# Performance work log

Measured on AMD Instinct MI355X. Metric: run time of the kernel, lower is better.

Reference implementation:

```python
import jax, jax.numpy as jnp
import numpy as np

NX, NY = 384, 384
H = 1e-4
DT = 5e-9
NT = 192
STRIDE = 4
RHO = 1610.0
F0 = 2.0e6
T0 = 4e-7
AMP = 1e10
GAUSS_A = 5e6

C11_INIT, C22_INIT, C12_INIT = 1.3074e11, 1.15e10, 1.049e10
C16_INIT, C26_INIT, C66_INIT = 3.067e10, 3.75e9, 1.477e10
B11 = (5e10, 2.5e11); B22 = (5e9, 5e10); B12 = (5e9, 5e10)
B16 = (0.0, 6e10); B26 = (0.0, 2e10); B66 = (5e9, 3e10)


def setup_inputs() -> dict:
    # log-parameter fields, constant-initialized as in the module __init__
    full = lambda v: jnp.full((1, NX, NY), np.log(v), dtype=jnp.float32)
    log_C11 = full(C11_INIT)
    log_C22 = full(C22_INIT)
    log_C12 = full(C12_INIT)
    log_C16 = full(abs(C16_INIT) + 1e6)
    log_C26 = full(abs(C26_INIT) + 1e6)
    log_C66 = full(C66_INIT)
    # Gaussian point-load distribution centered at domain center
    Lx, Ly = H * (NX - 1), H * (NY - 1)
    x = np.linspace(-Lx / 2, Lx / 2, NX)
    y = np.linspace(-Ly / 2, Ly / 2, NY)
    X, Y = np.meshgrid(x, y, indexing='ij')
    gauss = (GAUSS_A / np.pi) * np.exp(-GAUSS_A * (X ** 2 + Y ** 2))
    # Ricker wavelet source signal over nt steps
    t = np.arange(NT) * DT
    tau = t - T0
    pft2 = (np.pi * F0 * tau) ** 2
    sig = AMP * (1.0 - 2.0 * pft2) * np.exp(-pft2)
    return {
        'log_C11': log_C11, 'log_C12': log_C12, 'log_C16': log_C16,
        'log_C22': log_C22, 'log_C26': log_C26, 'log_C66': log_C66,
        'gaussian_dist': jnp.asarray(gauss, dtype=jnp.float32),
        'source_signal': jnp.asarray(sig, dtype=jnp.float32),
    }


def _stencils(u, hinv2):
    # u: (B, nx, ny). Zero padding == fixed (u=0) boundary, matching conv2d_fixed.
    up = jnp.pad(u, ((0, 0), (1, 1), (1, 1)))
    d2x = (up[:, :-2, 1:-1] - 2.0 * u + up[:, 2:, 1:-1]) * hinv2
    d2y = (up[:, 1:-1, :-2] - 2.0 * u + up[:, 1:-1, 2:]) * hinv2
    dxy = 0.25 * (up[:, :-2, :-2] - up[:, :-2, 2:] - up[:, 2:, :-2] + up[:, 2:, 2:]) * hinv2
    return d2x, d2y, dxy


def _simulate(log_C11, log_C12, log_C16, log_C22, log_C26, log_C66,
              gaussian_dist, source_signal):
    clip = lambda lc, b: jnp.clip(jnp.exp(lc), b[0], b[1])
    C11 = clip(log_C11, B11); C22 = clip(log_C22, B22); C12 = clip(log_C12, B12)
    C16 = clip(log_C16, B16); C26 = clip(log_C26, B26); C66 = clip(log_C66, B66)
    hinv2 = jnp.float32(1.0 / (H * H))
    dt2 = jnp.float32(DT * DT)
    g = gaussian_dist[None]  # (1, nx, ny)
    C12p66 = C12 + C66

    def step(carry, sig_t):
        ux1, uy1, ux2, uy2 = carry
        dxx_x, dyy_x, dxy_x = _stencils(ux1, hinv2)
        dxx_y, dyy_y, dxy_y = _stencils(uy1, hinv2)
        Lux = (C11 * dxx_x + C66 * dyy_x + C12p66 * dxy_y
               + 2.0 * C16 * dxy_x + C16 * dxx_y + C26 * dyy_y)
        Luy = (C66 * dxx_y + C22 * dyy_y + C12p66 * dxy_x
               + C16 * dxx_x + C26 * dyy_x + 2.0 * C26 * dxy_y)
        # Ricker point source on the y-component (source_component='y')
        ax = Lux / RHO
        ay = (Luy + sig_t * g) / RHO
        ux_new = 2.0 * ux1 - ux2 + dt2 * ax
        uy_new = 2.0 * uy1 - uy2 + dt2 * ay
        return (ux_new, uy_new, ux1, uy1), (ux_new, uy_new)

    z = jnp.zeros((1, NX, NY), dtype=jnp.float32)
    _, (ux_all, uy_all) = jax.lax.scan(step, (z, z, z, z), source_signal)
    # subsample by primary_time_stride -> (1, nt//stride, nx, ny)
    ux_f = jnp.transpose(ux_all[STRIDE - 1::STRIDE], (1, 0, 2, 3))
    uy_f = jnp.transpose(uy_all[STRIDE - 1::STRIDE], (1, 0, 2, 3))
    return jnp.stack([ux_f, uy_f])  # (2, 1, nt_out, nx, ny)


def reference(log_C11, log_C12, log_C16, log_C22, log_C26, log_C66,
              gaussian_dist, source_signal):
    return _simulate(log_C11, log_C12, log_C16, log_C22, log_C26, log_C66,
                     gaussian_dist, source_signal)
```

## Files before the change

### kernel.cpp

```cpp
#include <hip/hip_runtime.h>


typedef float v2f __attribute__((ext_vector_type(2)));

#define NXg 384
#define NYg 384
#define NPT (NXg * NYg)
#define NFRAMES 48

#define OWN 24
#define HALO 12
#define TS 48
#define KSTEPS 12
#define NLAUNCH 16

#define H_   1e-4
#define DT_  5e-9
#define RHO_ 1610.0

#define B11_LO 5e10f
#define B11_HI 2.5e11f
#define B22_LO 5e9f
#define B22_HI 5e10f
#define B12_LO 5e9f
#define B12_HI 5e10f
#define B16_LO 0.0f
#define B16_HI 6e10f
#define B26_LO 0.0f
#define B26_HI 2e10f
#define B66_LO 5e9f
#define B66_HI 3e10f

static __device__ __constant__ float kScale  = (float)(DT_ * DT_ / (H_ * H_) / RHO_);
static __device__ __constant__ float kSrcScl = (float)(DT_ * DT_ / RHO_);

__device__ __forceinline__ float clipf(float v, float lo, float hi) {
    return fminf(fmaxf(v, lo), hi);
}
__device__ __forceinline__ v2f vfma(v2f a, v2f b, v2f c) {
    return __builtin_elementwise_fma(a, b, c);
}
__device__ __forceinline__ v2f vbc(float s) { v2f r; r[0] = s; r[1] = s; return r; }


__global__ __launch_bounds__(256)
void setup_kernel(const float* __restrict__ lc11, const float* __restrict__ lc12,
                  const float* __restrict__ lc16, const float* __restrict__ lc22,
                  const float* __restrict__ lc26, const float* __restrict__ lc66,
                  const float* __restrict__ gauss, float* __restrict__ ws) {
    int i = blockIdx.x * blockDim.x + threadIdx.x;
    if (i >= NPT) return;
    float C11 = clipf(expf(lc11[i]), B11_LO, B11_HI);
    float C12 = clipf(expf(lc12[i]), B12_LO, B12_HI);
    float C16 = clipf(expf(lc16[i]), B16_LO, B16_HI);
    float C22 = clipf(expf(lc22[i]), B22_LO, B22_HI);
    float C26 = clipf(expf(lc26[i]), B26_LO, B26_HI);
    float C66 = clipf(expf(lc66[i]), B66_LO, B66_HI);
    float s = kScale;
    ws[0 * NPT + i] = C11 * s;
    ws[1 * NPT + i] = C22 * s;
    ws[2 * NPT + i] = (C12 + C66) * s;
    ws[3 * NPT + i] = C16 * s;
    ws[4 * NPT + i] = C26 * s;
    ws[5 * NPT + i] = C66 * s;
    ws[6 * NPT + i] = gauss[i] * kSrcScl;
    v2f* c0 = (v2f*)(ws + 7 * (size_t)NPT);
    v2f* o0 = c0 + NPT;
    c0[i] = vbc(0.0f);
    o0[i] = vbc(0.0f);
}

__global__ __launch_bounds__(256, 1)
void fused_kernel(const float* __restrict__ ws, const float* __restrict__ sig,
                  const v2f* __restrict__ inCur, const v2f* __restrict__ inOld,
                  v2f* __restrict__ outCur, v2f* __restrict__ outOld,
                  float* __restrict__ out, int L) {
    __shared__ v2f sb[2][TS][TS + 1];

    const int tid = threadIdx.x;
    const int tx = tid >> 4;
    const int ty = tid & 15;
    const int r0 = 3 * tx;
    const int c0 = 3 * ty;
    const int gx0 = blockIdx.y * OWN - HALO;
    const int gy0 = blockIdx.x * OWN - HALO;

    v2f cur[9], old_[9];
    float a11[9], a22[9], a12p66[9], a16[9], a26[9], a66[9], gs[9];
    int gidx[9];

#pragma unroll
    for (int i = 0; i < 3; ++i) {
#pragma unroll
        for (int j = 0; j < 3; ++j) {
            int p = i * 3 + j;
            int gx = gx0 + r0 + i;
            int gy = gy0 + c0 + j;
            bool d = (unsigned)gx < (unsigned)NXg && (unsigned)gy < (unsigned)NYg;
            int g = d ? gx * NYg + gy : 0;
            gidx[p] = g;
            cur[p]  = d ? inCur[g] : vbc(0.0f);
            old_[p] = d ? inOld[g] : vbc(0.0f);
            a11[p]    = d ? ws[0 * NPT + g] : 0.0f;
            a22[p]    = d ? ws[1 * NPT + g] : 0.0f;
            a12p66[p] = d ? ws[2 * NPT + g] : 0.0f;
            a16[p]    = d ? ws[3 * NPT + g] : 0.0f;
            a26[p]    = d ? ws[4 * NPT + g] : 0.0f;
            a66[p]    = d ? ws[5 * NPT + g] : 0.0f;
            gs[p]     = d ? ws[6 * NPT + g] : 0.0f;
        }
    }

    const int rm = (r0 > 0) ? r0 - 1 : 0;
    const int rp = (r0 + 3 < TS) ? r0 + 3 : TS - 1;
    const int cm = (c0 > 0) ? c0 - 1 : 0;
    const int cp = (c0 + 3 < TS) ? c0 + 3 : TS - 1;

    const bool owned = (tx >= 4) && (tx < 12) && (ty >= 4) && (ty < 12);
    const int t0 = L * KSTEPS;

#pragma unroll
    for (int i = 0; i < 3; ++i)
#pragma unroll
        for (int j = 0; j < 3; ++j)
            sb[0][r0 + i][c0 + j] = cur[i * 3 + j];
    __syncthreads();

#pragma unroll 1
    for (int s = 1; s <= KSTEPS; ++s) {
        const v2f (*rb)[TS + 1] = sb[(s - 1) & 1];
        v2f (*wb)[TS + 1] = sb[s & 1];
        const float sig_t = sig[t0 + s - 1];

        v2f v[5][5];
#pragma unroll
        for (int i = 0; i < 3; ++i)
#pragma unroll
            for (int j = 0; j < 3; ++j)
                v[i + 1][j + 1] = cur[i * 3 + j];
        v[0][0] = rb[rm][cm];  v[0][4] = rb[rm][cp];
        v[4][0] = rb[rp][cm];  v[4][4] = rb[rp][cp];
#pragma unroll
        for (int j = 0; j < 3; ++j) {
            v[0][j + 1] = rb[rm][c0 + j];
            v[4][j + 1] = rb[rp][c0 + j];
            v[j + 1][0] = rb[r0 + j][cm];
            v[j + 1][4] = rb[r0 + j][cp];
        }

        v2f dh[5][3];
#pragma unroll
        for (int i = 0; i < 5; ++i)
#pragma unroll
            for (int j = 0; j < 3; ++j)
                dh[i][j] = v[i][j + 2] - v[i][j];

        const v2f m2 = vbc(-2.0f);
        const v2f qt = vbc(0.25f);
#pragma unroll
        for (int i = 0; i < 3; ++i)
#pragma unroll
            for (int j = 0; j < 3; ++j) {
                int p = i * 3 + j;
                v2f c = v[i + 1][j + 1];
                v2f sxx = vfma(m2, c, v[i][j + 1] + v[i + 2][j + 1]);
                v2f syy = vfma(m2, c, v[i + 1][j] + v[i + 1][j + 2]);
                v2f sxy = qt * (dh[i + 2][j] - dh[i][j]);

                float lux = fmaf(a11[p], sxx[0],
                            fmaf(a66[p], syy[0],
                            fmaf(a12p66[p], sxy[1],
                            fmaf(a16[p], fmaf(2.0f, sxy[0], sxx[1]),
                                 a26[p] * syy[1]))));
                float luy = fmaf(a66[p], sxx[1],
                            fmaf(a22[p], syy[1],
                            fmaf(a12p66[p], sxy[0],
                            fmaf(a16[p], sxx[0],
                                 a26[p] * fmaf(2.0f, sxy[1], syy[0])))));

                float nx = fmaf(2.0f, c[0], lux) - old_[p][0];
                float ny = fmaf(2.0f, c[1], fmaf(sig_t, gs[p], luy)) - old_[p][1];
                old_[p] = c;
                v2f n; n[0] = nx; n[1] = ny;
                cur[p] = n;
            }

        if ((s & 3) == 0 && owned) {
            int f = 3 * L + (s >> 2) - 1;
            float* oux = out + (size_t)f * NPT;
            float* ouy = out + (size_t)(NFRAMES + f) * NPT;
#pragma unroll
            for (int p = 0; p < 9; ++p) {
                oux[gidx[p]] = cur[p][0];
                ouy[gidx[p]] = cur[p][1];
            }
        }

#pragma unroll
        for (int i = 0; i < 3; ++i)
#pragma unroll
            for (int j = 0; j < 3; ++j)
                wb[r0 + i][c0 + j] = cur[i * 3 + j];
        __syncthreads();
    }

    if (owned) {
#pragma unroll
        for (int p = 0; p < 9; ++p) {
            int g = gidx[p];
            outCur[g] = cur[p];
            outOld[g] = old_[p];
        }
    }
}

extern "C" void kernel_launch(void* const* d_in, const int* in_sizes, int n_in,
                              void* d_out, int out_size, void* d_ws, size_t ws_size,
                              hipStream_t stream) {
    const float* lc11  = (const float*)d_in[0];
    const float* lc12  = (const float*)d_in[1];
    const float* lc16  = (const float*)d_in[2];
    const float* lc22  = (const float*)d_in[3];
    const float* lc26  = (const float*)d_in[4];
    const float* lc66  = (const float*)d_in[5];
    const float* gauss = (const float*)d_in[6];
    const float* sig   = (const float*)d_in[7];

    float* ws  = (float*)d_ws;
    float* out = (float*)d_out;

    setup_kernel<<<(NPT + 255) / 256, 256, 0, stream>>>(lc11, lc12, lc16, lc22,
                                                        lc26, lc66, gauss, ws);

    v2f* set0c = (v2f*)(ws + 7 * (size_t)NPT);
    v2f* set0o = set0c + NPT;
    v2f* set1c = (v2f*)(ws + 11 * (size_t)NPT);
    v2f* set1o = set1c + NPT;

    dim3 grid(NXg / OWN, NYg / OWN);
    for (int L = 0; L < NLAUNCH; ++L) {
        v2f* ic = (L & 1) ? set1c : set0c;
        v2f* io = (L & 1) ? set1o : set0o;
        v2f* oc = (L & 1) ? set0c : set1c;
        v2f* oo = (L & 1) ? set0o : set1o;
        fused_kernel<<<grid, 256, 0, stream>>>(ws, sig, ic, io, oc, oo, out, L);
    }
}
```

Measured before the change: 363.6 us.

## Pack coefficients and state into float4 and vectorize the update with packed FMAs

```diff
diff --git a/kernel.cpp b/kernel.cpp
--- a/kernel.cpp
+++ b/kernel.cpp
@@ -41,6 +41,9 @@
     return __builtin_elementwise_fma(a, b, c);
 }
 __device__ __forceinline__ v2f vbc(float s) { v2f r; r[0] = s; r[1] = s; return r; }
+__device__ __forceinline__ v2f vswap(v2f a) { return __builtin_shufflevector(a, a, 1, 0); }
+
+#define LDS_BARRIER() asm volatile("s_waitcnt lgkmcnt(0)\n\ts_barrier" ::: "memory")
 
 
 __global__ __launch_bounds__(256)
@@ -57,23 +60,17 @@
     float C26 = clipf(expf(lc26[i]), B26_LO, B26_HI);
     float C66 = clipf(expf(lc66[i]), B66_LO, B66_HI);
     float s = kScale;
-    ws[0 * NPT + i] = C11 * s;
-    ws[1 * NPT + i] = C22 * s;
-    ws[2 * NPT + i] = (C12 + C66) * s;
-    ws[3 * NPT + i] = C16 * s;
-    ws[4 * NPT + i] = C26 * s;
-    ws[5 * NPT + i] = C66 * s;
-    ws[6 * NPT + i] = gauss[i] * kSrcScl;
-    v2f* c0 = (v2f*)(ws + 7 * (size_t)NPT);
-    v2f* o0 = c0 + NPT;
-    c0[i] = vbc(0.0f);
-    o0[i] = vbc(0.0f);
+    float4* C0 = (float4*)ws;
+    float4* C1 = (float4*)(ws + 4 * (size_t)NPT);
+    C0[i] = make_float4(C11 * s, C22 * s, (C12 + C66) * s, C16 * s);
+    C1[i] = make_float4(C26 * s, C66 * s, gauss[i] * kSrcScl, 0.0f);
+    float4* s0 = (float4*)(ws + 8 * (size_t)NPT);
+    s0[i] = make_float4(0.0f, 0.0f, 0.0f, 0.0f);
 }
 
 __global__ __launch_bounds__(256, 1)
 void fused_kernel(const float* __restrict__ ws, const float* __restrict__ sig,
-                  const v2f* __restrict__ inCur, const v2f* __restrict__ inOld,
-                  v2f* __restrict__ outCur, v2f* __restrict__ outOld,
+                  const float4* __restrict__ inS, float4* __restrict__ outS,
                   float* __restrict__ out, int L) {
     __shared__ v2f sb[2][TS][TS + 1];
 
@@ -85,8 +82,12 @@
     const int gx0 = blockIdx.y * OWN - HALO;
     const int gy0 = blockIdx.x * OWN - HALO;
 
+    const float4* __restrict__ C0 = (const float4*)ws;
+    const float4* __restrict__ C1 = (const float4*)(ws + 4 * (size_t)NPT);
+
     v2f cur[9], old_[9];
-    float a11[9], a22[9], a12p66[9], a16[9], a26[9], a66[9], gs[9];
+    v2f ca[9], cb[9];
+    float a12p66[9], a16[9], a26[9], gs[9];
     int gidx[9];
 
 #pragma unroll
@@ -99,17 +100,22 @@
             bool d = (unsigned)gx < (unsigned)NXg && (unsigned)gy < (unsigned)NYg;
             int g = d ? gx * NYg + gy : 0;
             gidx[p] = g;
-            cur[p]  = d ? inCur[g] : vbc(0.0f);
-            old_[p] = d ? inOld[g] : vbc(0.0f);
-            a11[p]    = d ? ws[0 * NPT + g] : 0.0f;
-            a22[p]    = d ? ws[1 * NPT + g] : 0.0f;
-            a12p66[p] = d ? ws[2 * NPT + g] : 0.0f;
-            a16[p]    = d ? ws[3 * NPT + g] : 0.0f;
-            a26[p]    = d ? ws[4 * NPT + g] : 0.0f;
-            a66[p]    = d ? ws[5 * NPT + g] : 0.0f;
-            gs[p]     = d ? ws[6 * NPT + g] : 0.0f;
-        }
-    }
+            float4 st = d ? inS[g] : make_float4(0, 0, 0, 0);
+            v2f c; c[0] = st.x; c[1] = st.y;
+            v2f o; o[0] = st.z; o[1] = st.w;
+            cur[p] = c; old_[p] = o;
+            float4 k0 = d ? C0[g] : make_float4(0, 0, 0, 0);
+            float4 k1 = d ? C1[g] : make_float4(0, 0, 0, 0);
+            v2f t; t[0] = k0.x; t[1] = k1.y; ca[p] = t;
+            v2f u; u[0] = k1.y; u[1] = k0.y; cb[p] = u;
+            a12p66[p] = k0.z; a16[p] = k0.w; a26[p] = k1.x; gs[p] = k1.z;
+        }
+    }
+
+    const int t0 = L * KSTEPS;
+    float sigv[KSTEPS];
+#pragma unroll
+    for (int k = 0; k < KSTEPS; ++k) sigv[k] = sig[t0 + k];
 
     const int rm = (r0 > 0) ? r0 - 1 : 0;
     const int rp = (r0 + 3 < TS) ? r0 + 3 : TS - 1;
@@ -117,20 +123,25 @@
     const int cp = (c0 + 3 < TS) ? c0 + 3 : TS - 1;
 
     const bool owned = (tx >= 4) && (tx < 12) && (ty >= 4) && (ty < 12);
-    const int t0 = L * KSTEPS;
 
 #pragma unroll
     for (int i = 0; i < 3; ++i)
 #pragma unroll
         for (int j = 0; j < 3; ++j)
             sb[0][r0 + i][c0 + j] = cur[i * 3 + j];
-    __syncthreads();
+    LDS_BARRIER();
+
+    v2f c20; c20[0] = 2.0f; c20[1] = 0.0f;
+    v2f c02; c02[0] = 0.0f; c02[1] = 2.0f;
+    const v2f m2 = vbc(-2.0f);
+    const v2f qt = vbc(0.25f);
+    const v2f two = vbc(2.0f);
 
 #pragma unroll 1
     for (int s = 1; s <= KSTEPS; ++s) {
         const v2f (*rb)[TS + 1] = sb[(s - 1) & 1];
         v2f (*wb)[TS + 1] = sb[s & 1];
-        const float sig_t = sig[t0 + s - 1];
+        v2f vsig; vsig[0] = 0.0f; vsig[1] = sigv[s - 1];
 
         v2f v[5][5];
 #pragma unroll
@@ -155,8 +166,6 @@
             for (int j = 0; j < 3; ++j)
                 dh[i][j] = v[i][j + 2] - v[i][j];
 
-        const v2f m2 = vbc(-2.0f);
-        const v2f qt = vbc(0.25f);
 #pragma unroll
         for (int i = 0; i < 3; ++i)
 #pragma unroll
@@ -167,21 +176,16 @@
                 v2f syy = vfma(m2, c, v[i + 1][j] + v[i + 1][j + 2]);
                 v2f sxy = qt * (dh[i + 2][j] - dh[i][j]);
 
-                float lux = fmaf(a11[p], sxx[0],
-                            fmaf(a66[p], syy[0],
-                            fmaf(a12p66[p], sxy[1],
-                            fmaf(a16[p], fmaf(2.0f, sxy[0], sxx[1]),
-                                 a26[p] * syy[1]))));
-                float luy = fmaf(a66[p], sxx[1],
-                            fmaf(a22[p], syy[1],
-                            fmaf(a12p66[p], sxy[0],
-                            fmaf(a16[p], sxx[0],
-                                 a26[p] * fmaf(2.0f, sxy[1], syy[0])))));
-
-                float nx = fmaf(2.0f, c[0], lux) - old_[p][0];
-                float ny = fmaf(2.0f, c[1], fmaf(sig_t, gs[p], luy)) - old_[p][1];
+                v2f t4 = vfma(c20, vbc(sxy[0]), vswap(sxx));
+                v2f t5 = vfma(c02, vbc(sxy[1]), vswap(syy));
+                v2f Lv = ca[p] * sxx;
+                Lv = vfma(cb[p], syy, Lv);
+                Lv = vfma(vbc(a12p66[p]), vswap(sxy), Lv);
+                Lv = vfma(vbc(a16[p]), t4, Lv);
+                Lv = vfma(vbc(a26[p]), t5, Lv);
+                Lv = vfma(vsig, vbc(gs[p]), Lv);
+                v2f n = vfma(two, c, Lv) - old_[p];
                 old_[p] = c;
-                v2f n; n[0] = nx; n[1] = ny;
                 cur[p] = n;
             }
 
@@ -201,15 +205,14 @@
 #pragma unroll
             for (int j = 0; j < 3; ++j)
                 wb[r0 + i][c0 + j] = cur[i * 3 + j];
-        __syncthreads();
+        LDS_BARRIER();
     }
 
     if (owned) {
 #pragma unroll
         for (int p = 0; p < 9; ++p) {
-            int g = gidx[p];
-            outCur[g] = cur[p];
-            outOld[g] = old_[p];
+            float4 st = make_float4(cur[p][0], cur[p][1], old_[p][0], old_[p][1]);
+            outS[gidx[p]] = st;
         }
     }
 }
@@ -232,17 +235,13 @@
     setup_kernel<<<(NPT + 255) / 256, 256, 0, stream>>>(lc11, lc12, lc16, lc22,
                                                         lc26, lc66, gauss, ws);
 
-    v2f* set0c = (v2f*)(ws + 7 * (size_t)NPT);
-    v2f* set0o = set0c + NPT;
-    v2f* set1c = (v2f*)(ws + 11 * (size_t)NPT);
-    v2f* set1o = set1c + NPT;
+    float4* set0 = (float4*)(ws + 8 * (size_t)NPT);
+    float4* set1 = (float4*)(ws + 12 * (size_t)NPT);
 
     dim3 grid(NXg / OWN, NYg / OWN);
     for (int L = 0; L < NLAUNCH; ++L) {
-        v2f* ic = (L & 1) ? set1c : set0c;
-        v2f* io = (L & 1) ? set1o : set0o;
-        v2f* oc = (L & 1) ? set0c : set1c;
-        v2f* oo = (L & 1) ? set0o : set1o;
-        fused_kernel<<<grid, 256, 0, stream>>>(ws, sig, ic, io, oc, oo, out, L);
-    }
-}
+        float4* iS = (L & 1) ? set1 : set0;
+        float4* oS = (L & 1) ? set0 : set1;
+        fused_kernel<<<grid, 256, 0, stream>>>(ws, sig, iS, oS, out, L);
+    }
+}
```

Result: faster. 353.7 us (-2.7%).
